# Optimization experiments

Hardware: AMD Instinct MI355X
Metric: run time of the kernel (lower is better)

Reference implementation:

```python
import jax, jax.numpy as jnp
import numpy as np

N = 50000      # nodes
E = 1600000    # edges per graph
IN = 64
HID = 64
OUT = 64


def _gat_conv(x, edge_index, W, a_src, a_dst, bias):
    """PyG GATConv, heads=1, add_self_loops=True, negative_slope=0.2."""
    n = x.shape[0]
    h = x @ W                                   # [N, d]
    loop = jnp.arange(n, dtype=edge_index.dtype)
    src = jnp.concatenate([edge_index[0], loop])
    dst = jnp.concatenate([edge_index[1], loop])
    e = jax.nn.leaky_relu((h @ a_src)[src] + (h @ a_dst)[dst], negative_slope=0.2)
    m = jax.ops.segment_max(e, dst, num_segments=n)          # stable edge-softmax per dst
    w = jnp.exp(e - m[dst])
    denom = jax.ops.segment_sum(w, dst, num_segments=n)
    alpha = w / denom[dst]                                   # [E+N]
    out = jax.ops.segment_sum(h[src] * alpha[:, None], dst, num_segments=n)
    return out + bias


def setup_inputs() -> dict:
    key = jax.random.key(0)
    ks = jax.random.split(key, 32)

    def glorot(k, shape):
        fan_out = shape[1] if len(shape) > 1 else 1
        lim = (6.0 / (shape[0] + fan_out)) ** 0.5
        return jax.random.uniform(k, shape, minval=-lim, maxval=lim, dtype=jnp.float32)

    inp = {
        "x_ind": jax.random.normal(ks[0], (N, IN), jnp.float32),
        "x_pos": jax.random.normal(ks[1], (N, IN), jnp.float32),
        "edge_ind": jax.random.randint(ks[2], (2, E), 0, N, dtype=jnp.int32),
        "edge_pos": jax.random.randint(ks[3], (2, E), 0, N, dtype=jnp.int32),
        "w1_ind": glorot(ks[4], (IN, HID)),
        "as1_ind": glorot(ks[5], (HID,)),
        "ad1_ind": glorot(ks[6], (HID,)),
        "b1_ind": jnp.zeros((HID,), jnp.float32),
        "w2_ind": glorot(ks[7], (HID, OUT)),
        "as2_ind": glorot(ks[8], (OUT,)),
        "ad2_ind": glorot(ks[9], (OUT,)),
        "b2_ind": jnp.zeros((OUT,), jnp.float32),
        "w1_pos": glorot(ks[10], (IN, HID)),
        "as1_pos": glorot(ks[11], (HID,)),
        "ad1_pos": glorot(ks[12], (HID,)),
        "b1_pos": jnp.zeros((HID,), jnp.float32),
        "w2_pos": glorot(ks[13], (HID, OUT)),
        "as2_pos": glorot(ks[14], (OUT,)),
        "ad2_pos": glorot(ks[15], (OUT,)),
        "b2_pos": jnp.zeros((OUT,), jnp.float32),
        "first_hop_att": glorot(ks[16], (2, HID)),
        "att_weight": glorot(ks[17], (2, OUT)),
        "mlp_w": glorot(ks[18], (OUT, 1)),
        "mlp_b": jnp.zeros((1,), jnp.float32),
    }
    return inp


def reference(x_ind, x_pos, edge_ind, edge_pos,
              w1_ind, as1_ind, ad1_ind, b1_ind,
              w2_ind, as2_ind, ad2_ind, b2_ind,
              w1_pos, as1_pos, ad1_pos, b1_pos,
              w2_pos, as2_pos, ad2_pos, b2_pos,
              first_hop_att, att_weight, mlp_w, mlp_b):
    h_i = jax.nn.relu(_gat_conv(x_ind, edge_ind, w1_ind, as1_ind, ad1_ind, b1_ind))
    h_p = jax.nn.relu(_gat_conv(x_pos, edge_pos, w1_pos, as1_pos, ad1_pos, b1_pos))
    # first-hop branch attention over the two graphs
    s1 = jnp.stack([jnp.sum(first_hop_att[0] * h_i, axis=1),
                    jnp.sum(first_hop_att[1] * h_p, axis=1)], axis=0)  # [2, N]
    a1 = jax.nn.softmax(s1, axis=0)
    fused = a1[0][:, None] * h_i + a1[1][:, None] * h_p
    g_i = _gat_conv(fused, edge_ind, w2_ind, as2_ind, ad2_ind, b2_ind)
    g_p = _gat_conv(fused, edge_pos, w2_pos, as2_pos, ad2_pos, b2_pos)
    s2 = jnp.stack([jnp.sum(att_weight[0] * g_i, axis=1),
                    jnp.sum(att_weight[1] * g_p, axis=1)], axis=0)
    a2 = jax.nn.softmax(s2, axis=0)
    x = a2[0][:, None] * g_i + a2[1][:, None] * g_p
    return x @ mlp_w + mlp_b                    # [N, 1]
```

## Files before the change

### kernel.cpp

```cpp
#include <hip/hip_runtime.h>
#include <hip/hip_fp16.h>

#define ND 64
#define BG 256
#define MAXB 512
#define PCH 16384
#define CAP 9216

__device__ __forceinline__ float lrelu(float x) { return x > 0.f ? x : 0.2f * x; }

__device__ __forceinline__ float wave_sum(float v) {
#pragma unroll
    for (int m = 32; m > 0; m >>= 1) v += __shfl_xor(v, m, 64);
    return v;
}

__device__ __forceinline__ void fma8(float* acc, float w, int4 raw) {
    union { int4 i; __half2 h[4]; } u;
    u.i = raw;
#pragma unroll
    for (int i = 0; i < 4; i++) {
        float2 f = __half22float2(u.h[i]);
        acc[2 * i]     = fmaf(w, f.x, acc[2 * i]);
        acc[2 * i + 1] = fmaf(w, f.y, acc[2 * i + 1]);
    }
}


__global__ void init_cursor(int* __restrict__ bcursor, int nb) {
    int t = threadIdx.x;
    if (t < nb) bcursor[t] = t * CAP;
}

__global__ void partition(const int* __restrict__ eI, const int* __restrict__ eP,
                          int* __restrict__ bcursor, int* __restrict__ part,
                          int N, int E, int nb) {
    __shared__ int hist[MAXB];
    __shared__ int lcur[MAXB];
    int t = threadIdx.x;
    int total = 2 * E;
    int chunkBase = blockIdx.x * PCH;
    int cnt = min(PCH, total - chunkBase);
    int cnt4 = cnt & ~3;
    if (t < nb) hist[t] = 0;
    __syncthreads();
    for (int i = t * 4; i < cnt4; i += 4096) {
        int e = chunkBase + i;
        int4 d; int base;
        if (e + 3 < E)   { d = *(const int4*)(eI + E + e); base = 0; }
        else if (e >= E) { d = *(const int4*)(eP + E + (e - E)); base = N; }
        else {
            int tmp[4];
#pragma unroll
            for (int k = 0; k < 4; k++) {
                int ee = e + k;
                tmp[k] = (ee < E) ? eI[E + ee] : N + eP[E + ee - E];
            }
            d = make_int4(tmp[0], tmp[1], tmp[2], tmp[3]); base = 0;
        }
        atomicAdd(&hist[(base + d.x) >> 8], 1);
        atomicAdd(&hist[(base + d.y) >> 8], 1);
        atomicAdd(&hist[(base + d.z) >> 8], 1);
        atomicAdd(&hist[(base + d.w) >> 8], 1);
    }
    for (int i = cnt4 + t; i < cnt; i += 1024) {
        int e = chunkBase + i;
        int idx = (e < E) ? eI[E + e] : N + eP[E + (e - E)];
        atomicAdd(&hist[idx >> 8], 1);
    }
    __syncthreads();
    if (t < nb) lcur[t] = hist[t] ? atomicAdd(&bcursor[t], hist[t]) : 0;
    __syncthreads();
    for (int i = t * 4; i < cnt4; i += 4096) {
        int e = chunkBase + i;
        int4 s4, d4; int base;
        if (e + 3 < E)   { s4 = *(const int4*)(eI + e); d4 = *(const int4*)(eI + E + e); base = 0; }
        else if (e >= E) { s4 = *(const int4*)(eP + (e - E)); d4 = *(const int4*)(eP + E + (e - E)); base = N; }
        else {
            int ts[4], td[4];
#pragma unroll
            for (int k = 0; k < 4; k++) {
                int ee = e + k;
                if (ee < E) { ts[k] = eI[ee]; td[k] = eI[E + ee]; }
                else        { ts[k] = eP[ee - E]; td[k] = N + eP[E + ee - E]; }
            }
            s4 = make_int4(ts[0], ts[1], ts[2], ts[3]);
            d4 = make_int4(td[0], td[1], td[2], td[3]); base = 0;
        }
        int idx, pos;
        idx = base + d4.x; pos = atomicAdd(&lcur[idx >> 8], 1); part[pos] = (s4.x << 8) | (idx & 255);
        idx = base + d4.y; pos = atomicAdd(&lcur[idx >> 8], 1); part[pos] = (s4.y << 8) | (idx & 255);
        idx = base + d4.z; pos = atomicAdd(&lcur[idx >> 8], 1); part[pos] = (s4.z << 8) | (idx & 255);
        idx = base + d4.w; pos = atomicAdd(&lcur[idx >> 8], 1); part[pos] = (s4.w << 8) | (idx & 255);
    }
    for (int i = cnt4 + t; i < cnt; i += 1024) {
        int e = chunkBase + i;
        int s, idx;
        if (e < E) { s = eI[e]; idx = eI[E + e]; }
        else       { s = eP[e - E]; idx = N + eP[E + (e - E)]; }
        int pos = atomicAdd(&lcur[idx >> 8], 1);
        part[pos] = (s << 8) | (idx & 255);
    }
}

__global__ void bucket_build(const int* __restrict__ part, const int* __restrict__ bcursor,
                             int* __restrict__ row, int* __restrict__ deg,
                             int* __restrict__ csr, int n2) {
    __shared__ int lhist[BG];
    __shared__ int lrow[BG];
    int b = blockIdx.x, t = threadIdx.x;
    int start = b * CAP;
    int cnt = bcursor[b] - start;
    int cnt4 = cnt & ~3;
    if (t < BG) lhist[t] = 0;
    __syncthreads();
    for (int j = t * 4; j < cnt4; j += 4096) {
        int4 p = *(const int4*)(part + start + j);
        atomicAdd(&lhist[p.x & 255], 1);
        atomicAdd(&lhist[p.y & 255], 1);
        atomicAdd(&lhist[p.z & 255], 1);
        atomicAdd(&lhist[p.w & 255], 1);
    }
    for (int j = cnt4 + t; j < cnt; j += 1024) atomicAdd(&lhist[part[start + j] & 255], 1);
    __syncthreads();
    int v = 0;
    if (t < BG) { v = lhist[t]; lrow[t] = v; }
    __syncthreads();
    for (int off = 1; off < BG; off <<= 1) {
        int a = (t < BG && t >= off) ? lrow[t - off] : 0;
        __syncthreads();
        if (t < BG) lrow[t] += a;
        __syncthreads();
    }
    if (t < BG) {
        int excl = lrow[t] - v;
        int g = b * BG + t;
        if (g < n2) { row[g] = start + excl; deg[g] = v; }
        lhist[t] = start + excl;
    }
    __syncthreads();
    for (int j = t * 4; j < cnt4; j += 4096) {
        int4 p = *(const int4*)(part + start + j);
        int pos;
        pos = atomicAdd(&lhist[p.x & 255], 1); csr[pos] = p.x >> 8;
        pos = atomicAdd(&lhist[p.y & 255], 1); csr[pos] = p.y >> 8;
        pos = atomicAdd(&lhist[p.z & 255], 1); csr[pos] = p.z >> 8;
        pos = atomicAdd(&lhist[p.w & 255], 1); csr[pos] = p.w >> 8;
    }
    for (int j = cnt4 + t; j < cnt; j += 1024) {
        int p = part[start + j];
        int pos = atomicAdd(&lhist[p & 255], 1);
        csr[pos] = p >> 8;
    }
}

__global__ void gemm_dual(const float* __restrict__ xA, const float* __restrict__ xB,
                          const float* __restrict__ WA, const float* __restrict__ WB,
                          const float* __restrict__ asA, const float* __restrict__ adA,
                          const float* __restrict__ asB, const float* __restrict__ adB,
                          __half* __restrict__ h16, float* __restrict__ ssrc,
                          float* __restrict__ sdst, int N) {
    int half = blockIdx.x & 1;
    int blk = blockIdx.x >> 1;
    int wave = threadIdx.x >> 6;
    int lane = threadIdx.x & 63;
    const float* x  = half ? xB : xA;
    const float* W  = half ? WB : WA;
    const float* av_ = half ? asB : asA;
    const float* dv_ = half ? adB : adA;
    int nodeBase = (blk * 4 + wave) * 4;
    __shared__ float xs[4][4 * ND];

    if (nodeBase + 3 < N) {
        *(float4*)&xs[wave][lane * 4] = *(const float4*)&x[(size_t)nodeBase * ND + lane * 4];
    } else if (nodeBase < N) {
#pragma unroll
        for (int i = 0; i < 4; i++) {
            int gi = nodeBase * ND + lane * 4 + i;
            xs[wave][lane * 4 + i] = (gi < N * ND) ? x[gi] : 0.f;
        }
    }
    __syncthreads();
    if (nodeBase >= N) return;

    float4 acc = {0.f, 0.f, 0.f, 0.f};
#pragma unroll
    for (int k = 0; k < ND; k++) {
        float wv = W[k * ND + lane];
        acc.x = fmaf(xs[wave][0 * ND + k], wv, acc.x);
        acc.y = fmaf(xs[wave][1 * ND + k], wv, acc.y);
        acc.z = fmaf(xs[wave][2 * ND + k], wv, acc.z);
        acc.w = fmaf(xs[wave][3 * ND + k], wv, acc.w);
    }
    float av = av_[lane], dv = dv_[lane];
    float s1x = wave_sum(acc.x * av), s2x = wave_sum(acc.x * dv);
    float s1y = wave_sum(acc.y * av), s2y = wave_sum(acc.y * dv);
    float s1z = wave_sum(acc.z * av), s2z = wave_sum(acc.z * dv);
    float s1w = wave_sum(acc.w * av), s2w = wave_sum(acc.w * dv);

    int g0 = half * N + nodeBase;
    h16[(size_t)(g0 + 0) * ND + lane] = __float2half(acc.x);
    if (nodeBase + 1 < N) h16[(size_t)(g0 + 1) * ND + lane] = __float2half(acc.y);
    if (nodeBase + 2 < N) h16[(size_t)(g0 + 2) * ND + lane] = __float2half(acc.z);
    if (nodeBase + 3 < N) h16[(size_t)(g0 + 3) * ND + lane] = __float2half(acc.w);
    if (lane == 0) {
        ssrc[g0] = s1x; sdst[g0] = s2x;
        if (nodeBase + 1 < N) { ssrc[g0 + 1] = s1y; sdst[g0 + 1] = s2y; }
        if (nodeBase + 2 < N) { ssrc[g0 + 2] = s1z; sdst[g0 + 2] = s2z; }
        if (nodeBase + 3 < N) { ssrc[g0 + 3] = s1w; sdst[g0 + 3] = s2w; }
    }
}

__global__ void aggregate_dual(const int* __restrict__ csr, const int* __restrict__ row,
                               const int* __restrict__ deg, const float* __restrict__ ssrc,
                               const float* __restrict__ sdst, const __half* __restrict__ h16,
                               const float* __restrict__ bA, const float* __restrict__ bB,
                               float* __restrict__ out, int N, int relu) {
    int half = blockIdx.x & 1;
    int wave = threadIdx.x >> 6;
    int lane = threadIdx.x & 63;
    int node = (blockIdx.x >> 1) * 4 + wave;
    if (node >= N) return;
    int g = half * N + node;
    const float* bias = half ? bB : bA;
    const float* ss = ssrc + (size_t)half * N;
    const __half* hh = h16 + (size_t)half * N * ND;

    int start = row[g];
    int end = start + deg[g];
    float sd = sdst[g];
    float wself = __expf(lrelu(ss[node] + sd));

    int group = lane >> 3;
    int fl8 = (lane & 7) * 8;
    float acc[8] = {0.f, 0.f, 0.f, 0.f, 0.f, 0.f, 0.f, 0.f};
    float denomp = 0.f;

    for (int base = start; base < end; base += 64) {
        int cnt = min(64, end - base);
        int sj = (lane < cnt) ? csr[base + lane] : 0;
        float wj = (lane < cnt) ? __expf(lrelu(ss[sj] + sd)) : 0.f;
        denomp += wj;
        int nq = (cnt + 7) >> 3;
        float w0 = __shfl(wj, group, 64);
        int s0 = __shfl(sj, group, 64);
        int4 raw0 = *(const int4*)(hh + (size_t)s0 * ND + fl8);
        for (int c = 1; c < nq; c++) {
            float w1 = __shfl(wj, c * 8 + group, 64);
            int s1 = __shfl(sj, c * 8 + group, 64);
            int4 raw1 = *(const int4*)(hh + (size_t)s1 * ND + fl8);
            fma8(acc, w0, raw0);
            w0 = w1; raw0 = raw1;
        }
        fma8(acc, w0, raw0);
    }

#pragma unroll
    for (int m = 8; m < 64; m <<= 1) {
#pragma unroll
        for (int i = 0; i < 8; i++) acc[i] += __shfl_xor(acc[i], m, 64);
    }
    float denom = wave_sum(denomp) + wself;

    int4 rawS = *(const int4*)(hh + (size_t)node * ND + fl8);
    union { int4 i; __half2 h[4]; } us;
    us.i = rawS;
    float v[8];
#pragma unroll
    for (int i = 0; i < 4; i++) {
        float2 f = __half22float2(us.h[i]);
        v[2 * i]     = (acc[2 * i]     + wself * f.x) / denom + bias[fl8 + 2 * i];
        v[2 * i + 1] = (acc[2 * i + 1] + wself * f.y) / denom + bias[fl8 + 2 * i + 1];
    }
    if (relu) {
#pragma unroll
        for (int i = 0; i < 8; i++) v[i] = fmaxf(v[i], 0.f);
    }
    if (lane < 8) {
        *(float4*)&out[(size_t)g * ND + fl8]     = make_float4(v[0], v[1], v[2], v[3]);
        *(float4*)&out[(size_t)g * ND + fl8 + 4] = make_float4(v[4], v[5], v[6], v[7]);
    }
}

__global__ void branch_att(const float* __restrict__ hbig, const float* __restrict__ att,
                           float* __restrict__ fused, int n) {
    int gid = blockIdx.x * blockDim.x + threadIdx.x;
    int node = gid >> 6, lane = gid & 63;
    if (node >= n) return;
    float vi = hbig[(size_t)node * ND + lane];
    float vp = hbig[((size_t)n + node) * ND + lane];
    float s0 = wave_sum(att[lane] * vi);
    float s1 = wave_sum(att[ND + lane] * vp);
    float m = fmaxf(s0, s1);
    float a0 = __expf(s0 - m), a1 = __expf(s1 - m);
    fused[(size_t)node * ND + lane] = (a0 * vi + a1 * vp) / (a0 + a1);
}

__global__ void branch_att_mlp(const float* __restrict__ hbig, const float* __restrict__ att,
                               const float* __restrict__ mlpw, const float* __restrict__ mlpb,
                               float* __restrict__ out, int n) {
    int gid = blockIdx.x * blockDim.x + threadIdx.x;
    int node = gid >> 6, lane = gid & 63;
    if (node >= n) return;
    float vi = hbig[(size_t)node * ND + lane];
    float vp = hbig[((size_t)n + node) * ND + lane];
    float s0 = wave_sum(att[lane] * vi);
    float s1 = wave_sum(att[ND + lane] * vp);
    float m = fmaxf(s0, s1);
    float a0 = __expf(s0 - m), a1 = __expf(s1 - m);
    float xj = (a0 * vi + a1 * vp) / (a0 + a1);
    float o = wave_sum(xj * mlpw[lane]);
    if (lane == 0) out[node] = o + mlpb[0];
}

extern "C" void kernel_launch(void* const* d_in, const int* in_sizes, int n_in,
                              void* d_out, int out_size, void* d_ws, size_t ws_size,
                              hipStream_t stream) {
    const int N = in_sizes[0] / ND;
    const int E = in_sizes[2] / 2;

    const float* x_ind = (const float*)d_in[0];
    const float* x_pos = (const float*)d_in[1];
    const int*   e_ind = (const int*)d_in[2];
    const int*   e_pos = (const int*)d_in[3];
    const float* w1i = (const float*)d_in[4];
    const float* as1i = (const float*)d_in[5];
    const float* ad1i = (const float*)d_in[6];
    const float* b1i = (const float*)d_in[7];
    const float* w2i = (const float*)d_in[8];
    const float* as2i = (const float*)d_in[9];
    const float* ad2i = (const float*)d_in[10];
    const float* b2i = (const float*)d_in[11];
    const float* w1p = (const float*)d_in[12];
    const float* as1p = (const float*)d_in[13];
    const float* ad1p = (const float*)d_in[14];
    const float* b1p = (const float*)d_in[15];
    const float* w2p = (const float*)d_in[16];
    const float* as2p = (const float*)d_in[17];
    const float* ad2p = (const float*)d_in[18];
    const float* b2p = (const float*)d_in[19];
    const float* fha = (const float*)d_in[20];
    const float* attw = (const float*)d_in[21];
    const float* mlpw = (const float*)d_in[22];
    const float* mlpb = (const float*)d_in[23];

    char* ws = (char*)d_ws;
    size_t off = 0;
    auto alloc = [&](size_t elems) { void* p = ws + off; off += elems * 4; return p; };

    const int n2 = 2 * N;
    const int nb = (n2 + BG - 1) / BG;

    __half* h16 = (__half*)alloc((size_t)n2 * ND / 2);
    float* hbig = (float*)alloc((size_t)n2 * ND);
    float* bufC = (float*)alloc((size_t)N * ND);
    float* ssrc = (float*)alloc(n2);
    float* sdst = (float*)alloc(n2);
    int* deg    = (int*)alloc(n2);
    int* rowi   = (int*)alloc(n2);
    int* csr    = (int*)alloc((size_t)nb * CAP);
    int* bcursor= (int*)alloc(MAXB);
    int* part   = (int*)hbig;

    const int gemmBlocks = 2 * ((N + 15) / 16);
    const int aggBlocks  = 2 * ((N + 3) / 4);
    const int nodeBlocks = (N + 3) / 4;
    const int partBlocks = (2 * E + PCH - 1) / PCH;

    init_cursor<<<1, 512, 0, stream>>>(bcursor, nb);
    partition<<<partBlocks, 1024, 0, stream>>>(e_ind, e_pos, bcursor, part, N, E, nb);
    bucket_build<<<nb, 1024, 0, stream>>>(part, bcursor, rowi, deg, csr, n2);

    gemm_dual<<<gemmBlocks, 256, 0, stream>>>(x_ind, x_pos, w1i, w1p,
                                              as1i, ad1i, as1p, ad1p,
                                              h16, ssrc, sdst, N);
    aggregate_dual<<<aggBlocks, 256, 0, stream>>>(csr, rowi, deg, ssrc, sdst, h16,
                                                  b1i, b1p, hbig, N, 1);
    branch_att<<<nodeBlocks, 256, 0, stream>>>(hbig, fha, bufC, N);

    gemm_dual<<<gemmBlocks, 256, 0, stream>>>(bufC, bufC, w2i, w2p,
                                              as2i, ad2i, as2p, ad2p,
                                              h16, ssrc, sdst, N);
    aggregate_dual<<<aggBlocks, 256, 0, stream>>>(csr, rowi, deg, ssrc, sdst, h16,
                                                  b2i, b2p, hbig, N, 0);
    branch_att_mlp<<<nodeBlocks, 256, 0, stream>>>(hbig, attw, mlpw, mlpb,
                                                   (float*)d_out, N);
}
```

Measured before the change: 371.5 us.

## Process four nodes per wavefront in GAT aggregation using 16-lane subgroups

Aggregation previously assigned one 64-lane wavefront per destination node, so with about 32 edges per node most lanes idled or did redundant reductions. Now each wavefront handles four nodes, each with a 16-lane subgroup that gathers two neighbors per step across eight feature lanes. The cross-lane reductions shrink to within the subgroup, and the grid is cut by a factor of four. Per-node edge lists shorter than 16 leave some lanes idle, and the serial dependency chain per subgroup becomes longer.

```diff
diff --git a/kernel.cpp b/kernel.cpp
--- a/kernel.cpp
+++ b/kernel.cpp
@@ -219,35 +219,38 @@
     int half = blockIdx.x & 1;
     int wave = threadIdx.x >> 6;
     int lane = threadIdx.x & 63;
-    int node = (blockIdx.x >> 1) * 4 + wave;
-    if (node >= N) return;
+    int sub  = lane >> 4;
+    int l16  = lane & 15;
+    int slot = l16 >> 3;
+    int fl8  = (l16 & 7) * 8;
+    int node = ((blockIdx.x >> 1) * 4 + wave) * 4 + sub;
+    bool valid = node < N;
     int g = half * N + node;
     const float* bias = half ? bB : bA;
     const float* ss = ssrc + (size_t)half * N;
     const __half* hh = h16 + (size_t)half * N * ND;
 
-    int start = row[g];
-    int end = start + deg[g];
-    float sd = sdst[g];
-    float wself = __expf(lrelu(ss[node] + sd));
-
-    int group = lane >> 3;
-    int fl8 = (lane & 7) * 8;
+    int start = valid ? row[g] : 0;
+    int cnt   = valid ? deg[g] : 0;
+    float sd  = valid ? sdst[g] : 0.f;
+    float wself = valid ? __expf(lrelu(ss[node] + sd)) : 0.f;
+
     float acc[8] = {0.f, 0.f, 0.f, 0.f, 0.f, 0.f, 0.f, 0.f};
     float denomp = 0.f;
-
-    for (int base = start; base < end; base += 64) {
-        int cnt = min(64, end - base);
-        int sj = (lane < cnt) ? csr[base + lane] : 0;
-        float wj = (lane < cnt) ? __expf(lrelu(ss[sj] + sd)) : 0.f;
+    int waveBase = sub << 4;
+
+    for (int base = 0; base < cnt; base += 16) {
+        int c16 = min(16, cnt - base);
+        int sj = (l16 < c16) ? csr[start + base + l16] : 0;
+        float wj = (l16 < c16) ? __expf(lrelu(ss[sj] + sd)) : 0.f;
         denomp += wj;
-        int nq = (cnt + 7) >> 3;
-        float w0 = __shfl(wj, group, 64);
-        int s0 = __shfl(sj, group, 64);
+        int nq = (c16 + 1) >> 1;
+        float w0 = __shfl(wj, waveBase + slot, 64);
+        int s0 = __shfl(sj, waveBase + slot, 64);
         int4 raw0 = *(const int4*)(hh + (size_t)s0 * ND + fl8);
         for (int c = 1; c < nq; c++) {
-            float w1 = __shfl(wj, c * 8 + group, 64);
-            int s1 = __shfl(sj, c * 8 + group, 64);
+            float w1 = __shfl(wj, waveBase + c * 2 + slot, 64);
+            int s1 = __shfl(sj, waveBase + c * 2 + slot, 64);
             int4 raw1 = *(const int4*)(hh + (size_t)s1 * ND + fl8);
             fma8(acc, w0, raw0);
             w0 = w1; raw0 = raw1;
@@ -256,12 +259,12 @@
     }
 
 #pragma unroll
-    for (int m = 8; m < 64; m <<= 1) {
-#pragma unroll
-        for (int i = 0; i < 8; i++) acc[i] += __shfl_xor(acc[i], m, 64);
-    }
-    float denom = wave_sum(denomp) + wself;
-
+    for (int i = 0; i < 8; i++) acc[i] += __shfl_xor(acc[i], 8, 64);
+#pragma unroll
+    for (int m = 1; m <= 8; m <<= 1) denomp += __shfl_xor(denomp, m, 64);
+    float denom = denomp + wself;
+
+    if (!valid || slot != 0) return;
     int4 rawS = *(const int4*)(hh + (size_t)node * ND + fl8);
     union { int4 i; __half2 h[4]; } us;
     us.i = rawS;
@@ -276,10 +279,8 @@
 #pragma unroll
         for (int i = 0; i < 8; i++) v[i] = fmaxf(v[i], 0.f);
     }
-    if (lane < 8) {
-        *(float4*)&out[(size_t)g * ND + fl8]     = make_float4(v[0], v[1], v[2], v[3]);
-        *(float4*)&out[(size_t)g * ND + fl8 + 4] = make_float4(v[4], v[5], v[6], v[7]);
-    }
+    *(float4*)&out[(size_t)g * ND + fl8]     = make_float4(v[0], v[1], v[2], v[3]);
+    *(float4*)&out[(size_t)g * ND + fl8 + 4] = make_float4(v[4], v[5], v[6], v[7]);
 }
 
 __global__ void branch_att(const float* __restrict__ hbig, const float* __restrict__ att,
@@ -363,7 +364,7 @@
     int* part   = (int*)hbig;
 
     const int gemmBlocks = 2 * ((N + 15) / 16);
-    const int aggBlocks  = 2 * ((N + 3) / 4);
+    const int aggBlocks  = 2 * ((N + 15) / 16);
     const int nodeBlocks = (N + 3) / 4;
     const int partBlocks = (2 * E + PCH - 1) / PCH;
 
```

After: 351.7 us. 1.06x faster.
